# Optimization experiments

Measured on AMD Instinct MI355X. Metric: run time of the kernel, lower is better.

Reference implementation:

```python
import jax, jax.numpy as jnp
import numpy as np

T, B, D, H = 4096, 4, 1024, 16


def setup_inputs() -> dict:
    key = jax.random.key(0)
    k0, k1, k2 = jax.random.split(key, 3)
    x = jax.random.normal(k0, (T, B, D), jnp.float32)
    Wqkv = jax.random.normal(k1, (3 * D, D), jnp.float32) * 0.02
    bqkv = jnp.zeros((3 * D,), jnp.float32)
    Wout = jax.random.normal(k2, (D, D), jnp.float32) * 0.02
    bout = jnp.zeros((D,), jnp.float32)
    return {"x": x, "Wqkv": Wqkv, "bqkv": bqkv, "Wout": Wout, "bout": bout, "nhead": H}


def reference(x, Wqkv, bqkv, Wout, bout, nhead):
    # x: (T, B, D) seq-first, query is key is value
    T_, B_, D_ = x.shape
    hd = D_ // nhead
    qkv = x @ Wqkv.T + bqkv                      # (T, B, 3D)
    q, k, v = jnp.split(qkv, 3, axis=-1)         # each (T, B, D)

    def heads(t):                                 # -> (B, H, T, hd)
        return t.reshape(T_, B_, nhead, hd).transpose(1, 2, 0, 3)

    q, k, v = heads(q), heads(k), heads(v)

    # Pearson correlation over the sequence axis: X, Y are (B, H, hd, T)
    X = jnp.swapaxes(q, -2, -1)
    Y = jnp.swapaxes(k, -2, -1)
    Xc = X - X.mean(-1, keepdims=True)
    Yc = Y - Y.mean(-1, keepdims=True)
    c = jnp.einsum('bhdt,bhet->bhde', Xc, Yc)    # (B, H, hd, hd)
    sx = (Xc ** 2).sum(-1)                       # (B, H, hd)
    sy = (Yc ** 2).sum(-1)                       # (B, H, hd)
    std = jnp.sqrt(sx[..., :, None] * sy[..., None, :])
    corr = jnp.clip(c / std, -1.0, 1.0)          # (B, H, hd, hd)

    attn = jnp.einsum('bhtd,bhde->bhte', v, corr)  # v @ corr: (B, H, T, hd)
    out = attn.transpose(2, 0, 1, 3).reshape(T_, B_, D_)  # (T, B, D)
    return out @ Wout.T + bout
```

## Files before the change

### kernel.cpp

```cpp
#include <hip/hip_runtime.h>
#include <hip/hip_bf16.h>

#define TDIM 4096
#define BDIM 4
#define DDIM 1024
#define HDIM 16
#define HD   64
#define MDIM (TDIM * BDIM)

typedef __attribute__((ext_vector_type(8))) short short8v;
typedef __attribute__((ext_vector_type(4))) float f32x4;

__device__ __forceinline__ ushort f2bfu(float f) {
  union { __hip_bfloat16 h; ushort u; } c;
  c.h = __float2bfloat16(f);
  return c.u;
}
__device__ __forceinline__ float bfu2f(ushort u) {
  union { ushort u; __hip_bfloat16 h; } c;
  c.u = u;
  return __bfloat162float(c.h);
}

#define GLOAD16(gp, lp) __builtin_amdgcn_global_load_lds( \
    (const __attribute__((address_space(1))) void*)(gp),  \
    (__attribute__((address_space(3))) void*)(lp), 16, 0, 0)

#define SWZ(row) (((row) >> 1) & 3)

__global__ __launch_bounds__(256)
void split_f32(const float* __restrict__ in, ushort* __restrict__ hi,
               ushort* __restrict__ lo, int n4)
{
  int i = blockIdx.x * blockDim.x + threadIdx.x;
  const int stride = gridDim.x * blockDim.x;
  for (; i < n4; i += stride) {
    const float4 v = ((const float4*)in)[i];
    ushort4 h, l;
    h.x = f2bfu(v.x); l.x = f2bfu(v.x - bfu2f(h.x));
    h.y = f2bfu(v.y); l.y = f2bfu(v.y - bfu2f(h.y));
    h.z = f2bfu(v.z); l.z = f2bfu(v.z - bfu2f(h.z));
    h.w = f2bfu(v.w); l.w = f2bfu(v.w - bfu2f(h.w));
    ((ushort4*)hi)[i] = h;
    ((ushort4*)lo)[i] = l;
  }
}

__global__ __launch_bounds__(256, 2)
void gemm1_mfma(const float* __restrict__ X, const ushort* __restrict__ Wh,
                const ushort* __restrict__ Wl, const float* __restrict__ bias,
                float* __restrict__ Qc, float* __restrict__ Kc,
                ushort* __restrict__ Vh, ushort* __restrict__ Vl)
{
  __shared__ ushort sAh[128][32], sAl[128][32], sBh[128][32], sBl[128][32];
  const int tid = threadIdx.x;
  const int lane = tid & 63, wid = tid >> 6;
  const int m0 = blockIdx.y * 128, n0 = blockIdx.x * 128;
  const int ar = tid >> 3, aq = tid & 7;
  const int wm = wid >> 1, wn = wid & 1;
  const int fr = lane & 15, kg = lane >> 4;

  f32x4 acc[4][4];
#pragma unroll
  for (int m = 0; m < 4; ++m)
#pragma unroll
    for (int n = 0; n < 4; ++n) acc[m][n] = (f32x4){0.f, 0.f, 0.f, 0.f};

  for (int k0 = 0; k0 < DDIM; k0 += 32) {
    float4 av[4];
#pragma unroll
    for (int i = 0; i < 4; ++i)
      av[i] = *(const float4*)&X[(size_t)(m0 + ar + i * 32) * DDIM + k0 + aq * 4];
#pragma unroll
    for (int j = 0; j < 4; ++j) {
      const int c = wid * 4 + j;
      const int r0 = (c & 7) * 16;
      const int row = r0 + (lane >> 2);
      const int s = lane & 3;
      const size_t goff = (size_t)(n0 + row) * DDIM + k0 + ((s ^ SWZ(row)) << 3);
      if (c < 8) GLOAD16(Wh + goff, &sBh[r0][0]);
      else       GLOAD16(Wl + goff, &sBl[r0][0]);
    }
#pragma unroll
    for (int i = 0; i < 4; ++i) {
      const int row = ar + i * 32;
      const int sl = (((aq >> 1) ^ SWZ(row)) << 3) + ((aq & 1) << 2);
      ushort4 hv, lv;
      hv.x = f2bfu(av[i].x); lv.x = f2bfu(av[i].x - bfu2f(hv.x));
      hv.y = f2bfu(av[i].y); lv.y = f2bfu(av[i].y - bfu2f(hv.y));
      hv.z = f2bfu(av[i].z); lv.z = f2bfu(av[i].z - bfu2f(hv.z));
      hv.w = f2bfu(av[i].w); lv.w = f2bfu(av[i].w - bfu2f(hv.w));
      *(ushort4*)&sAh[row][sl] = hv;
      *(ushort4*)&sAl[row][sl] = lv;
    }
    __syncthreads();

    short8v ah[4], al[4], bh[4], bl[4];
#pragma unroll
    for (int m = 0; m < 4; ++m) {
      const int row = wm * 64 + m * 16 + fr;
      const int so = (kg ^ SWZ(row)) << 3;
      ah[m] = *(const short8v*)&sAh[row][so];
      al[m] = *(const short8v*)&sAl[row][so];
    }
#pragma unroll
    for (int n = 0; n < 4; ++n) {
      const int col = wn * 64 + n * 16 + fr;
      const int so = (kg ^ SWZ(col)) << 3;
      bh[n] = *(const short8v*)&sBh[col][so];
      bl[n] = *(const short8v*)&sBl[col][so];
    }
#pragma unroll
    for (int m = 0; m < 4; ++m)
#pragma unroll
      for (int n = 0; n < 4; ++n) {
        acc[m][n] = __builtin_amdgcn_mfma_f32_16x16x32_bf16(ah[m], bh[n], acc[m][n], 0, 0, 0);
        acc[m][n] = __builtin_amdgcn_mfma_f32_16x16x32_bf16(ah[m], bl[n], acc[m][n], 0, 0, 0);
        acc[m][n] = __builtin_amdgcn_mfma_f32_16x16x32_bf16(al[m], bh[n], acc[m][n], 0, 0, 0);
      }
    __syncthreads();
  }

  const int region = n0 >> 10;
#pragma unroll
  for (int m = 0; m < 4; ++m)
#pragma unroll
    for (int n = 0; n < 4; ++n) {
      const int col = n0 + wn * 64 + n * 16 + fr;
      const float bz = bias[col];
      const int cc = col & 1023;
      const int hh = cc >> 6, dd = cc & 63;
#pragma unroll
      for (int r = 0; r < 4; ++r) {
        const int row = m0 + wm * 64 + m * 16 + kg * 4 + r;
        const float v = acc[m][n][r] + bz;
        const int t = row >> 2, b = row & 3;
        const size_t ho = (((size_t)(b * 16 + hh)) * 4096 + t) * 64 + dd;
        if (region == 0)      Qc[ho] = v;
        else if (region == 1) Kc[ho] = v;
        else {
          const size_t o = (size_t)row * 1024 + cc;
          const ushort h2 = f2bfu(v);
          Vh[o] = h2;
          Vl[o] = f2bfu(v - bfu2f(h2));
        }
      }
    }
}

__global__ __launch_bounds__(256, 2)
void gemm2_mfma(const ushort* __restrict__ Vh, const ushort* __restrict__ Vl,
                const ushort* __restrict__ Weh, const ushort* __restrict__ Wel,
                const float* __restrict__ bias, float* __restrict__ Out)
{
  __shared__ ushort sAh[64][32], sAl[64][32], sBh[128][32], sBl[128][32];
  const int tid = threadIdx.x;
  const int lane = tid & 63, wid = tid >> 6;
  const int m0 = blockIdx.y * 64, n0 = blockIdx.x * 128, bb = blockIdx.z;
  const int wm = wid >> 1, wn = wid & 1;
  const int fr = lane & 15, kg = lane >> 4;

  f32x4 acc[2][4];
#pragma unroll
  for (int m = 0; m < 2; ++m)
#pragma unroll
    for (int n = 0; n < 4; ++n) acc[m][n] = (f32x4){0.f, 0.f, 0.f, 0.f};

  const size_t wB = (size_t)bb * DDIM * DDIM;

  for (int k0 = 0; k0 < DDIM; k0 += 32) {
#pragma unroll
    for (int j = 0; j < 6; ++j) {
      const int c = wid * 6 + j;
      const int rl = lane >> 2, s = lane & 3;
      if (c < 8) {
        const int r0 = (c & 3) * 16;
        const int row = r0 + rl;
        const size_t g = (size_t)((m0 + row) * 4 + bb) * 1024 + k0 + ((s ^ SWZ(row)) << 3);
        if (c < 4) GLOAD16(Vh + g, &sAh[r0][0]);
        else       GLOAD16(Vl + g, &sAl[r0][0]);
      } else {
        const int r0 = ((c - 8) & 7) * 16;
        const int row = r0 + rl;
        const size_t g = wB + (size_t)(n0 + row) * 1024 + k0 + ((s ^ SWZ(row)) << 3);
        if (c < 16) GLOAD16(Weh + g, &sBh[r0][0]);
        else        GLOAD16(Wel + g, &sBl[r0][0]);
      }
    }
    __syncthreads();

    short8v ah[2], al[2], bh[4], bl[4];
#pragma unroll
    for (int m = 0; m < 2; ++m) {
      const int row = wm * 32 + m * 16 + fr;
      const int so = (kg ^ SWZ(row)) << 3;
      ah[m] = *(const short8v*)&sAh[row][so];
      al[m] = *(const short8v*)&sAl[row][so];
    }
#pragma unroll
    for (int n = 0; n < 4; ++n) {
      const int col = wn * 64 + n * 16 + fr;
      const int so = (kg ^ SWZ(col)) << 3;
      bh[n] = *(const short8v*)&sBh[col][so];
      bl[n] = *(const short8v*)&sBl[col][so];
    }
#pragma unroll
    for (int m = 0; m < 2; ++m)
#pragma unroll
      for (int n = 0; n < 4; ++n) {
        acc[m][n] = __builtin_amdgcn_mfma_f32_16x16x32_bf16(ah[m], bh[n], acc[m][n], 0, 0, 0);
        acc[m][n] = __builtin_amdgcn_mfma_f32_16x16x32_bf16(ah[m], bl[n], acc[m][n], 0, 0, 0);
        acc[m][n] = __builtin_amdgcn_mfma_f32_16x16x32_bf16(al[m], bh[n], acc[m][n], 0, 0, 0);
      }
    __syncthreads();
  }

  float* Ob = Out + (size_t)bb * 1024;
#pragma unroll
  for (int m = 0; m < 2; ++m)
#pragma unroll
    for (int n = 0; n < 4; ++n) {
      const int col = n0 + wn * 64 + n * 16 + fr;
      const float bz = bias[col];
#pragma unroll
      for (int r = 0; r < 4; ++r) {
        const int row = m0 + wm * 32 + m * 16 + kg * 4 + r;
        Ob[(size_t)row * 4096 + col] = acc[m][n][r] + bz;
      }
    }
}

__global__ __launch_bounds__(256)
void corr_partial(const float* __restrict__ Qc, const float* __restrict__ Kc,
                  float* __restrict__ P)
{
  __shared__ float qs[4][16][64];
  __shared__ float ks[4][16][64];
  __shared__ float ssum[4][4][64];
  const int bh  = blockIdx.x;
  const int seg = blockIdx.y;
  const int tid = threadIdx.x;
  const int wid = tid >> 6, lane = tid & 63;
  const float* qb = Qc + (size_t)bh * 262144;
  const float* kb = Kc + (size_t)bh * 262144;
  const int ty = lane >> 3;
  const int tx = lane & 7;
  const int rr = lane >> 4;
  const int cq = lane & 15;

  float acc[8][8];
#pragma unroll
  for (int i = 0; i < 8; ++i)
#pragma unroll
    for (int j = 0; j < 8; ++j) acc[i][j] = 0.f;
  float sQ[4]  = {0,0,0,0}, sK[4]  = {0,0,0,0};
  float sQ2[4] = {0,0,0,0}, sK2[4] = {0,0,0,0};

  for (int c = 0; c < 4; ++c) {
    const int tbase = seg * 256 + wid * 64 + c * 16;
    float4 qv[4], kv[4];
#pragma unroll
    for (int i = 0; i < 4; ++i) {
      const size_t g = (size_t)(tbase + rr + i*4) * 64 + cq * 4;
      qv[i] = *(const float4*)&qb[g];
      kv[i] = *(const float4*)&kb[g];
    }
#pragma unroll
    for (int i = 0; i < 4; ++i) {
      const int row = rr + i*4;
      *(float4*)&qs[wid][row][cq*4] = qv[i];
      *(float4*)&ks[wid][row][cq*4] = kv[i];
      sQ[0] += qv[i].x; sQ[1] += qv[i].y; sQ[2] += qv[i].z; sQ[3] += qv[i].w;
      sK[0] += kv[i].x; sK[1] += kv[i].y; sK[2] += kv[i].z; sK[3] += kv[i].w;
      sQ2[0] = fmaf(qv[i].x, qv[i].x, sQ2[0]); sQ2[1] = fmaf(qv[i].y, qv[i].y, sQ2[1]);
      sQ2[2] = fmaf(qv[i].z, qv[i].z, sQ2[2]); sQ2[3] = fmaf(qv[i].w, qv[i].w, sQ2[3]);
      sK2[0] = fmaf(kv[i].x, kv[i].x, sK2[0]); sK2[1] = fmaf(kv[i].y, kv[i].y, sK2[1]);
      sK2[2] = fmaf(kv[i].z, kv[i].z, sK2[2]); sK2[3] = fmaf(kv[i].w, kv[i].w, sK2[3]);
    }
#pragma unroll 8
    for (int t = 0; t < 16; ++t) {
      const float4 qa  = *(const float4*)&qs[wid][t][ty*8];
      const float4 qb4 = *(const float4*)&qs[wid][t][ty*8+4];
      const float4 ka  = *(const float4*)&ks[wid][t][tx*8];
      const float4 kb4 = *(const float4*)&ks[wid][t][tx*8+4];
      const float av[8] = {qa.x, qa.y, qa.z, qa.w, qb4.x, qb4.y, qb4.z, qb4.w};
      const float bv[8] = {ka.x, ka.y, ka.z, ka.w, kb4.x, kb4.y, kb4.z, kb4.w};
#pragma unroll
      for (int i = 0; i < 8; ++i)
#pragma unroll
        for (int j = 0; j < 8; ++j)
          acc[i][j] = fmaf(av[i], bv[j], acc[i][j]);
    }
  }

#pragma unroll
  for (int j = 0; j < 4; ++j) {
    sQ[j]  += __shfl_xor(sQ[j], 16, 64);  sQ[j]  += __shfl_xor(sQ[j], 32, 64);
    sK[j]  += __shfl_xor(sK[j], 16, 64);  sK[j]  += __shfl_xor(sK[j], 32, 64);
    sQ2[j] += __shfl_xor(sQ2[j], 16, 64); sQ2[j] += __shfl_xor(sQ2[j], 32, 64);
    sK2[j] += __shfl_xor(sK2[j], 16, 64); sK2[j] += __shfl_xor(sK2[j], 32, 64);
  }
  if (lane < 16) {
    float4 q4; q4.x = sQ[0];  q4.y = sQ[1];  q4.z = sQ[2];  q4.w = sQ[3];
    float4 k4; k4.x = sK[0];  k4.y = sK[1];  k4.z = sK[2];  k4.w = sK[3];
    float4 q2; q2.x = sQ2[0]; q2.y = sQ2[1]; q2.z = sQ2[2]; q2.w = sQ2[3];
    float4 k2; k2.x = sK2[0]; k2.y = sK2[1]; k2.z = sK2[2]; k2.w = sK2[3];
    *(float4*)&ssum[wid][0][lane*4] = q4;
    *(float4*)&ssum[wid][1][lane*4] = k4;
    *(float4*)&ssum[wid][2][lane*4] = q2;
    *(float4*)&ssum[wid][3][lane*4] = k2;
  }

  float* cbuf = &qs[0][0][0];
  __syncthreads();
#pragma unroll
  for (int w = 0; w < 4; ++w) {
    if (wid == w) {
#pragma unroll
      for (int i = 0; i < 8; ++i) {
        float* p0 = &cbuf[(ty*8 + i) * 64 + tx*8];
        if (w == 0) {
          float4 o0, o1;
          o0.x = acc[i][0]; o0.y = acc[i][1]; o0.z = acc[i][2]; o0.w = acc[i][3];
          o1.x = acc[i][4]; o1.y = acc[i][5]; o1.z = acc[i][6]; o1.w = acc[i][7];
          *(float4*)p0 = o0; *(float4*)(p0 + 4) = o1;
        } else {
          float4 o0 = *(const float4*)p0, o1 = *(const float4*)(p0 + 4);
          o0.x += acc[i][0]; o0.y += acc[i][1]; o0.z += acc[i][2]; o0.w += acc[i][3];
          o1.x += acc[i][4]; o1.y += acc[i][5]; o1.z += acc[i][6]; o1.w += acc[i][7];
          *(float4*)p0 = o0; *(float4*)(p0 + 4) = o1;
        }
      }
    }
    __syncthreads();
  }

  float* Pb = P + (size_t)(bh * 16 + seg) * 4352;
#pragma unroll
  for (int i = 0; i < 4; ++i)
    ((float4*)Pb)[tid + 256*i] = ((const float4*)cbuf)[tid + 256*i];
  {
    const int comp = tid >> 6, d = tid & 63;
    Pb[4096 + tid] = ssum[0][comp][d] + ssum[1][comp][d] +
                     ssum[2][comp][d] + ssum[3][comp][d];
  }
}

__global__ __launch_bounds__(256)
void corr_finalize(const float* __restrict__ P, float* __restrict__ corr)
{
  __shared__ float fin[4][64];
  const int bh = blockIdx.x, qtr = blockIdx.y;
  const int tid = threadIdx.x;
  const float* Pb = P + (size_t)bh * 16 * 4352;

  float s = 0.f;
  for (int seg = 0; seg < 16; ++seg) s += Pb[(size_t)seg*4352 + 4096 + tid];
  fin[tid >> 6][tid & 63] = s;

  float cacc[4] = {0.f, 0.f, 0.f, 0.f};
  for (int seg = 0; seg < 16; ++seg) {
#pragma unroll
    for (int i = 0; i < 4; ++i)
      cacc[i] += Pb[(size_t)seg*4352 + qtr*1024 + tid + i*256];
  }
  __syncthreads();

  const float invT = 1.0f / (float)TDIM;
#pragma unroll
  for (int i = 0; i < 4; ++i) {
    const int f = qtr*1024 + tid + i*256;
    const int d = f >> 6, e = f & 63;
    const float sq = fin[0][d], sk = fin[1][e];
    const float sq2 = fin[2][d], sk2 = fin[3][e];
    const float cc = cacc[i] - sq * sk * invT;
    const float sx = sq2 - sq * sq * invT;
    const float sy = sk2 - sk * sk * invT;
    float v = cc / sqrtf(sx * sy);
    v = fminf(1.f, fmaxf(-1.f, v));
    corr[(size_t)bh * 4096 + f] = v;
  }
}

__global__ __launch_bounds__(256)
void weff_kernel(const float* __restrict__ corr, const float* __restrict__ Wout,
                 ushort* __restrict__ Weh, ushort* __restrict__ Wel)
{
  __shared__ float cs[64][64];
  __shared__ float ws[128][64];
  const int bh = blockIdx.x;
  const int b = bh >> 4, h = bh & 15;
  const int n0 = blockIdx.y * 128;
  const int tid = threadIdx.x;

  const float* cb = corr + (size_t)bh * 4096;
  float4* csv = (float4*)&cs[0][0];
#pragma unroll
  for (int i = 0; i < 4; ++i)
    csv[tid + 256*i] = ((const float4*)cb)[tid + 256*i];

  const int wr = tid >> 1, wh = (tid & 1) * 32;
  const float* wrow = Wout + (size_t)(n0 + wr) * DDIM + h * HD + wh;
#pragma unroll
  for (int i = 0; i < 8; ++i)
    *(float4*)&ws[wr][wh + i*4] = *(const float4*)&wrow[i*4];
  __syncthreads();

  const int ni = (tid >> 3) * 4;
  const int di = (tid & 7) * 8;
  float acc[4][8];
#pragma unroll
  for (int i = 0; i < 4; ++i)
#pragma unroll
    for (int j = 0; j < 8; ++j) acc[i][j] = 0.f;

  for (int e = 0; e < 64; ++e) {
    float wv[4], cv[8];
#pragma unroll
    for (int i = 0; i < 4; ++i) wv[i] = ws[ni + i][e];
#pragma unroll
    for (int j = 0; j < 8; ++j) cv[j] = cs[di + j][e];
#pragma unroll
    for (int i = 0; i < 4; ++i)
#pragma unroll
      for (int j = 0; j < 8; ++j)
        acc[i][j] = fmaf(wv[i], cv[j], acc[i][j]);
  }

  const size_t base = (size_t)b * DDIM * DDIM + h * HD;
#pragma unroll
  for (int i = 0; i < 4; ++i) {
    ushort4 h0, l0, h1, l1;
    h0.x = f2bfu(acc[i][0]); l0.x = f2bfu(acc[i][0] - bfu2f(h0.x));
    h0.y = f2bfu(acc[i][1]); l0.y = f2bfu(acc[i][1] - bfu2f(h0.y));
    h0.z = f2bfu(acc[i][2]); l0.z = f2bfu(acc[i][2] - bfu2f(h0.z));
    h0.w = f2bfu(acc[i][3]); l0.w = f2bfu(acc[i][3] - bfu2f(h0.w));
    h1.x = f2bfu(acc[i][4]); l1.x = f2bfu(acc[i][4] - bfu2f(h1.x));
    h1.y = f2bfu(acc[i][5]); l1.y = f2bfu(acc[i][5] - bfu2f(h1.y));
    h1.z = f2bfu(acc[i][6]); l1.z = f2bfu(acc[i][6] - bfu2f(h1.z));
    h1.w = f2bfu(acc[i][7]); l1.w = f2bfu(acc[i][7] - bfu2f(h1.w));
    const size_t o = base + (size_t)(n0 + ni + i) * DDIM + di;
    *(ushort4*)&Weh[o]     = h0;
    *(ushort4*)&Weh[o + 4] = h1;
    *(ushort4*)&Wel[o]     = l0;
    *(ushort4*)&Wel[o + 4] = l1;
  }
}

extern "C" void kernel_launch(void* const* d_in, const int* in_sizes, int n_in,
                              void* d_out, int out_size, void* d_ws, size_t ws_size,
                              hipStream_t stream)
{
  (void)in_sizes; (void)n_in; (void)out_size; (void)ws_size;
  const float* x    = (const float*)d_in[0];
  const float* Wqkv = (const float*)d_in[1];
  const float* bqkv = (const float*)d_in[2];
  const float* Wout = (const float*)d_in[3];
  const float* bout = (const float*)d_in[4];
  float* out = (float*)d_out;

  char* w = (char*)d_ws;
  float*  Qc    = (float*)w;   w += (size_t)67108864;
  float*  Kc    = (float*)w;   w += (size_t)67108864;
  ushort* Vh    = (ushort*)w;  w += (size_t)33554432;
  ushort* Vl    = (ushort*)w;  w += (size_t)33554432;
  float*  corrB = (float*)w;   w += (size_t)1048576;
  char* R1 = w;                w += (size_t)17825792;
  char* R2 = w;
  ushort* Wqh   = (ushort*)R1;
  ushort* Wql   = Wqh + (size_t)3145728;
  float*  P     = (float*)R1;
  ushort* Weh   = (ushort*)R2;
  ushort* Wel   = Weh + (size_t)4194304;

  split_f32<<<dim3(1024), 256, 0, stream>>>(Wqkv, Wqh, Wql, 786432);
  gemm1_mfma<<<dim3(24, 128), 256, 0, stream>>>(x, Wqh, Wql, bqkv, Qc, Kc, Vh, Vl);
  corr_partial<<<dim3(64, 16), 256, 0, stream>>>(Qc, Kc, P);
  corr_finalize<<<dim3(64, 4), 256, 0, stream>>>(P, corrB);
  weff_kernel<<<dim3(64, 8), 256, 0, stream>>>(corrB, Wout, Weh, Wel);
  gemm2_mfma<<<dim3(8, 64, 4), 256, 0, stream>>>(Vh, Vl, Weh, Wel, bout, out);
}
```

Measured before the change: 638.6 us.

## Pre-split X to bf16 hi/lo and process QKV GEMM in two halves

X is converted to bf16 hi/lo once by a separate kernel, so the first GEMM can stream A tiles straight into LDS with asynchronous global-to-LDS loads instead of loading fp32 and splitting in registers. The GEMM and correlation-partial stage now run in two halves of the sequence, reusing half-size Q/K buffers, which halves that workspace and may keep more of it cache-resident. The trailing barrier moves to the top of the k-loop. The cost is an extra pass over X in memory plus an extra kernel launch, and two serialized half-size launches.

```diff
diff --git a/kernel.cpp b/kernel.cpp
--- a/kernel.cpp
+++ b/kernel.cpp
@@ -47,16 +47,16 @@
 }
 
 __global__ __launch_bounds__(256, 2)
-void gemm1_mfma(const float* __restrict__ X, const ushort* __restrict__ Wh,
-                const ushort* __restrict__ Wl, const float* __restrict__ bias,
+void gemm1_mfma(const ushort* __restrict__ Xh, const ushort* __restrict__ Xl,
+                const ushort* __restrict__ Wh, const ushort* __restrict__ Wl,
+                const float* __restrict__ bias,
                 float* __restrict__ Qc, float* __restrict__ Kc,
-                ushort* __restrict__ Vh, ushort* __restrict__ Vl)
+                ushort* __restrict__ Vh, ushort* __restrict__ Vl, int mbase)
 {
   __shared__ ushort sAh[128][32], sAl[128][32], sBh[128][32], sBl[128][32];
   const int tid = threadIdx.x;
   const int lane = tid & 63, wid = tid >> 6;
-  const int m0 = blockIdx.y * 128, n0 = blockIdx.x * 128;
-  const int ar = tid >> 3, aq = tid & 7;
+  const int m0 = mbase + blockIdx.y * 128, n0 = blockIdx.x * 128;
   const int wm = wid >> 1, wn = wid & 1;
   const int fr = lane & 15, kg = lane >> 4;
 
@@ -67,31 +67,18 @@
     for (int n = 0; n < 4; ++n) acc[m][n] = (f32x4){0.f, 0.f, 0.f, 0.f};
 
   for (int k0 = 0; k0 < DDIM; k0 += 32) {
-    float4 av[4];
-#pragma unroll
-    for (int i = 0; i < 4; ++i)
-      av[i] = *(const float4*)&X[(size_t)(m0 + ar + i * 32) * DDIM + k0 + aq * 4];
-#pragma unroll
-    for (int j = 0; j < 4; ++j) {
-      const int c = wid * 4 + j;
+    __syncthreads();
+#pragma unroll
+    for (int j = 0; j < 8; ++j) {
+      const int c = wid * 8 + j;
       const int r0 = (c & 7) * 16;
       const int row = r0 + (lane >> 2);
       const int s = lane & 3;
-      const size_t goff = (size_t)(n0 + row) * DDIM + k0 + ((s ^ SWZ(row)) << 3);
-      if (c < 8) GLOAD16(Wh + goff, &sBh[r0][0]);
-      else       GLOAD16(Wl + goff, &sBl[r0][0]);
-    }
-#pragma unroll
-    for (int i = 0; i < 4; ++i) {
-      const int row = ar + i * 32;
-      const int sl = (((aq >> 1) ^ SWZ(row)) << 3) + ((aq & 1) << 2);
-      ushort4 hv, lv;
-      hv.x = f2bfu(av[i].x); lv.x = f2bfu(av[i].x - bfu2f(hv.x));
-      hv.y = f2bfu(av[i].y); lv.y = f2bfu(av[i].y - bfu2f(hv.y));
-      hv.z = f2bfu(av[i].z); lv.z = f2bfu(av[i].z - bfu2f(hv.z));
-      hv.w = f2bfu(av[i].w); lv.w = f2bfu(av[i].w - bfu2f(hv.w));
-      *(ushort4*)&sAh[row][sl] = hv;
-      *(ushort4*)&sAl[row][sl] = lv;
+      const int ks = k0 + ((s ^ SWZ(row)) << 3);
+      if (c < 8)       GLOAD16(Xh + (size_t)(m0 + row) * DDIM + ks, &sAh[r0][0]);
+      else if (c < 16) GLOAD16(Xl + (size_t)(m0 + row) * DDIM + ks, &sAl[r0][0]);
+      else if (c < 24) GLOAD16(Wh + (size_t)(n0 + row) * DDIM + ks, &sBh[r0][0]);
+      else             GLOAD16(Wl + (size_t)(n0 + row) * DDIM + ks, &sBl[r0][0]);
     }
     __syncthreads();
 
@@ -118,7 +105,6 @@
         acc[m][n] = __builtin_amdgcn_mfma_f32_16x16x32_bf16(ah[m], bl[n], acc[m][n], 0, 0, 0);
         acc[m][n] = __builtin_amdgcn_mfma_f32_16x16x32_bf16(al[m], bh[n], acc[m][n], 0, 0, 0);
       }
-    __syncthreads();
   }
 
   const int region = n0 >> 10;
@@ -134,8 +120,8 @@
       for (int r = 0; r < 4; ++r) {
         const int row = m0 + wm * 64 + m * 16 + kg * 4 + r;
         const float v = acc[m][n][r] + bz;
-        const int t = row >> 2, b = row & 3;
-        const size_t ho = (((size_t)(b * 16 + hh)) * 4096 + t) * 64 + dd;
+        const int tl = (row - mbase) >> 2, b = row & 3;
+        const size_t ho = (((size_t)(b * 16 + hh)) * 2048 + tl) * 64 + dd;
         if (region == 0)      Qc[ho] = v;
         else if (region == 1) Kc[ho] = v;
         else {
@@ -232,7 +218,7 @@
 
 __global__ __launch_bounds__(256)
 void corr_partial(const float* __restrict__ Qc, const float* __restrict__ Kc,
-                  float* __restrict__ P)
+                  float* __restrict__ P, int segbase)
 {
   __shared__ float qs[4][16][64];
   __shared__ float ks[4][16][64];
@@ -241,8 +227,8 @@
   const int seg = blockIdx.y;
   const int tid = threadIdx.x;
   const int wid = tid >> 6, lane = tid & 63;
-  const float* qb = Qc + (size_t)bh * 262144;
-  const float* kb = Kc + (size_t)bh * 262144;
+  const float* qb = Qc + (size_t)bh * 131072;
+  const float* kb = Kc + (size_t)bh * 131072;
   const int ty = lane >> 3;
   const int tx = lane & 7;
   const int rr = lane >> 4;
@@ -335,7 +321,7 @@
     __syncthreads();
   }
 
-  float* Pb = P + (size_t)(bh * 16 + seg) * 4352;
+  float* Pb = P + (size_t)(bh * 16 + segbase + seg) * 4352;
 #pragma unroll
   for (int i = 0; i < 4; ++i)
     ((float4*)Pb)[tid + 256*i] = ((const float4*)cbuf)[tid + 256*i];
@@ -460,22 +446,28 @@
   float* out = (float*)d_out;
 
   char* w = (char*)d_ws;
-  float*  Qc    = (float*)w;   w += (size_t)67108864;
-  float*  Kc    = (float*)w;   w += (size_t)67108864;
+  ushort* Xh    = (ushort*)w;  w += (size_t)33554432;
+  ushort* Xl    = (ushort*)w;  w += (size_t)33554432;
+  float*  Qch   = (float*)w;   w += (size_t)33554432;
+  float*  Kch   = (float*)w;   w += (size_t)33554432;
   ushort* Vh    = (ushort*)w;  w += (size_t)33554432;
   ushort* Vl    = (ushort*)w;  w += (size_t)33554432;
   float*  corrB = (float*)w;   w += (size_t)1048576;
-  char* R1 = w;                w += (size_t)17825792;
+  float*  P     = (float*)w;   w += (size_t)17825792;
   char* R2 = w;
-  ushort* Wqh   = (ushort*)R1;
+  ushort* Wqh   = (ushort*)R2;
   ushort* Wql   = Wqh + (size_t)3145728;
-  float*  P     = (float*)R1;
   ushort* Weh   = (ushort*)R2;
   ushort* Wel   = Weh + (size_t)4194304;
 
+  split_f32<<<dim3(2048), 256, 0, stream>>>(x, Xh, Xl, 4194304);
   split_f32<<<dim3(1024), 256, 0, stream>>>(Wqkv, Wqh, Wql, 786432);
-  gemm1_mfma<<<dim3(24, 128), 256, 0, stream>>>(x, Wqh, Wql, bqkv, Qc, Kc, Vh, Vl);
-  corr_partial<<<dim3(64, 16), 256, 0, stream>>>(Qc, Kc, P);
+  gemm1_mfma<<<dim3(24, 64), 256, 0, stream>>>(Xh, Xl, Wqh, Wql, bqkv,
+                                               Qch, Kch, Vh, Vl, 0);
+  corr_partial<<<dim3(64, 8), 256, 0, stream>>>(Qch, Kch, P, 0);
+  gemm1_mfma<<<dim3(24, 64), 256, 0, stream>>>(Xh, Xl, Wqh, Wql, bqkv,
+                                               Qch, Kch, Vh, Vl, 8192);
+  corr_partial<<<dim3(64, 8), 256, 0, stream>>>(Qch, Kch, P, 8);
   corr_finalize<<<dim3(64, 4), 256, 0, stream>>>(P, corrB);
   weff_kernel<<<dim3(64, 8), 256, 0, stream>>>(corrB, Wout, Weh, Wel);
   gemm2_mfma<<<dim3(8, 64, 4), 256, 0, stream>>>(Vh, Vl, Weh, Wel, bout, out);
```

Result: slower. 705.1 us (+10.4%).

## Double-buffer LDS tiles in QKV projection GEMM to overlap loads with MFMA

Applied to the files above, without the earlier changes.

The QKV projection GEMM now keeps two LDS buffers for the A (split bf16 hi/lo) and B tiles. It issues the global-to-LDS loads and X register loads for the next k-step before running the MFMAs on the current buffer, then converts and stores the next A tile afterwards. This drops one barrier per iteration and hides global memory latency behind compute. In exchange it doubles LDS use to 64KB per block, which may limit the two blocks per CU requested by launch bounds, and raises register pressure from the prefetched float4 values.

```diff
diff --git a/kernel.cpp b/kernel.cpp
--- a/kernel.cpp
+++ b/kernel.cpp
@@ -52,7 +52,8 @@
                 float* __restrict__ Qc, float* __restrict__ Kc,
                 ushort* __restrict__ Vh, ushort* __restrict__ Vl)
 {
-  __shared__ ushort sAh[128][32], sAl[128][32], sBh[128][32], sBl[128][32];
+  __shared__ ushort sAh[2][128][32], sAl[2][128][32];
+  __shared__ ushort sBh[2][128][32], sBl[2][128][32];
   const int tid = threadIdx.x;
   const int lane = tid & 63, wid = tid >> 6;
   const int m0 = blockIdx.y * 128, n0 = blockIdx.x * 128;
@@ -66,20 +67,20 @@
 #pragma unroll
     for (int n = 0; n < 4; ++n) acc[m][n] = (f32x4){0.f, 0.f, 0.f, 0.f};
 
-  for (int k0 = 0; k0 < DDIM; k0 += 32) {
+  {
     float4 av[4];
 #pragma unroll
     for (int i = 0; i < 4; ++i)
-      av[i] = *(const float4*)&X[(size_t)(m0 + ar + i * 32) * DDIM + k0 + aq * 4];
+      av[i] = *(const float4*)&X[(size_t)(m0 + ar + i * 32) * DDIM + aq * 4];
 #pragma unroll
     for (int j = 0; j < 4; ++j) {
       const int c = wid * 4 + j;
       const int r0 = (c & 7) * 16;
       const int row = r0 + (lane >> 2);
       const int s = lane & 3;
-      const size_t goff = (size_t)(n0 + row) * DDIM + k0 + ((s ^ SWZ(row)) << 3);
-      if (c < 8) GLOAD16(Wh + goff, &sBh[r0][0]);
-      else       GLOAD16(Wl + goff, &sBl[r0][0]);
+      const size_t goff = (size_t)(n0 + row) * DDIM + ((s ^ SWZ(row)) << 3);
+      if (c < 8) GLOAD16(Wh + goff, &sBh[0][r0][0]);
+      else       GLOAD16(Wl + goff, &sBl[0][r0][0]);
     }
 #pragma unroll
     for (int i = 0; i < 4; ++i) {
@@ -90,25 +91,47 @@
       hv.y = f2bfu(av[i].y); lv.y = f2bfu(av[i].y - bfu2f(hv.y));
       hv.z = f2bfu(av[i].z); lv.z = f2bfu(av[i].z - bfu2f(hv.z));
       hv.w = f2bfu(av[i].w); lv.w = f2bfu(av[i].w - bfu2f(hv.w));
-      *(ushort4*)&sAh[row][sl] = hv;
-      *(ushort4*)&sAl[row][sl] = lv;
+      *(ushort4*)&sAh[0][row][sl] = hv;
+      *(ushort4*)&sAl[0][row][sl] = lv;
     }
     __syncthreads();
+  }
+
+  int cur = 0;
+  for (int k0 = 0; k0 < DDIM; k0 += 32) {
+    const int nxt = cur ^ 1;
+    const bool has_next = (k0 + 32 < DDIM);
+    float4 av[4];
+    if (has_next) {
+#pragma unroll
+      for (int j = 0; j < 4; ++j) {
+        const int c = wid * 4 + j;
+        const int r0 = (c & 7) * 16;
+        const int row = r0 + (lane >> 2);
+        const int s = lane & 3;
+        const size_t goff = (size_t)(n0 + row) * DDIM + k0 + 32 + ((s ^ SWZ(row)) << 3);
+        if (c < 8) GLOAD16(Wh + goff, &sBh[nxt][r0][0]);
+        else       GLOAD16(Wl + goff, &sBl[nxt][r0][0]);
+      }
+#pragma unroll
+      for (int i = 0; i < 4; ++i)
+        av[i] = *(const float4*)&X[(size_t)(m0 + ar + i * 32) * DDIM + k0 + 32 + aq * 4];
+    }
 
     short8v ah[4], al[4], bh[4], bl[4];
 #pragma unroll
     for (int m = 0; m < 4; ++m) {
       const int row = wm * 64 + m * 16 + fr;
       const int so = (kg ^ SWZ(row)) << 3;
-      ah[m] = *(const short8v*)&sAh[row][so];
-      al[m] = *(const short8v*)&sAl[row][so];
+      ah[m] = *(const short8v*)&sAh[cur][row][so];
+      al[m] = *(const short8v*)&sAl[cur][row][so];
     }
 #pragma unroll
     for (int n = 0; n < 4; ++n) {
       const int col = wn * 64 + n * 16 + fr;
       const int so = (kg ^ SWZ(col)) << 3;
-      bh[n] = *(const short8v*)&sBh[col][so];
-      bl[n] = *(const short8v*)&sBl[col][so];
+      bh[n] = *(const short8v*)&sBh[cur][col][so];
+      bl[n] = *(const short8v*)&sBl[cur][col][so];
     }
 #pragma unroll
     for (int m = 0; m < 4; ++m)
@@ -118,7 +141,23 @@
         acc[m][n] = __builtin_amdgcn_mfma_f32_16x16x32_bf16(ah[m], bl[n], acc[m][n], 0, 0, 0);
         acc[m][n] = __builtin_amdgcn_mfma_f32_16x16x32_bf16(al[m], bh[n], acc[m][n], 0, 0, 0);
       }
+
+    if (has_next) {
+#pragma unroll
+      for (int i = 0; i < 4; ++i) {
+        const int row = ar + i * 32;
+        const int sl = (((aq >> 1) ^ SWZ(row)) << 3) + ((aq & 1) << 2);
+        ushort4 hv, lv;
+        hv.x = f2bfu(av[i].x); lv.x = f2bfu(av[i].x - bfu2f(hv.x));
+        hv.y = f2bfu(av[i].y); lv.y = f2bfu(av[i].y - bfu2f(hv.y));
+        hv.z = f2bfu(av[i].z); lv.z = f2bfu(av[i].z - bfu2f(hv.z));
+        hv.w = f2bfu(av[i].w); lv.w = f2bfu(av[i].w - bfu2f(hv.w));
+        *(ushort4*)&sAh[nxt][row][sl] = hv;
+        *(ushort4*)&sAl[nxt][row][sl] = lv;
+      }
+    }
     __syncthreads();
+    cur = nxt;
   }
 
   const int region = n0 >> 10;
```

After: 665.8 us. 4.3% more time.

## Fold V projection into per-batch output weight to skip V materialization

Applied to the files above, without the earlier changes.

Stops computing and storing V in the first GEMM. Instead the value projection weight is composed with the per-batch effective output weight (Wout·corr), giving a fused per-batch weight Wfull and bias. The final GEMM then reads x directly, with a 128-row tile and on-the-fly bf16 hi/lo splitting. This removes a third of GEMM1's work and the V write/read round trip, at the cost of an extra 4×1024³ weight-composition GEMM, a small serial bias kernel, and an extra rounding step in the fused weights.

```diff
diff --git a/kernel.cpp b/kernel.cpp
--- a/kernel.cpp
+++ b/kernel.cpp
@@ -46,11 +46,42 @@
   }
 }
 
+__global__ __launch_bounds__(256)
+void wvt_split(const float* __restrict__ Wqkv, ushort* __restrict__ WvTh,
+               ushort* __restrict__ WvTl)
+{
+  __shared__ float ld[64][68];
+  const int d0 = blockIdx.x * 64, e0 = blockIdx.y * 64;
+  const int tid = threadIdx.x;
+  const int rr = tid >> 4, cc = tid & 15;
+#pragma unroll
+  for (int i = 0; i < 4; ++i) {
+    const int el = rr + i * 16;
+    const float4 v = *(const float4*)&Wqkv[(size_t)(2048 + e0 + el) * 1024 + d0 + cc * 4];
+    ld[el][cc*4+0] = v.x; ld[el][cc*4+1] = v.y;
+    ld[el][cc*4+2] = v.z; ld[el][cc*4+3] = v.w;
+  }
+  __syncthreads();
+#pragma unroll
+  for (int i = 0; i < 4; ++i) {
+    const int dl = rr + i * 16;
+    const float v0 = ld[cc*4+0][dl], v1 = ld[cc*4+1][dl];
+    const float v2 = ld[cc*4+2][dl], v3 = ld[cc*4+3][dl];
+    ushort4 h4, l4;
+    h4.x = f2bfu(v0); l4.x = f2bfu(v0 - bfu2f(h4.x));
+    h4.y = f2bfu(v1); l4.y = f2bfu(v1 - bfu2f(h4.y));
+    h4.z = f2bfu(v2); l4.z = f2bfu(v2 - bfu2f(h4.z));
+    h4.w = f2bfu(v3); l4.w = f2bfu(v3 - bfu2f(h4.w));
+    const size_t o = (size_t)(d0 + dl) * 1024 + e0 + cc * 4;
+    *(ushort4*)&WvTh[o] = h4;
+    *(ushort4*)&WvTl[o] = l4;
+  }
+}
+
 __global__ __launch_bounds__(256, 2)
-void gemm1_mfma(const float* __restrict__ X, const ushort* __restrict__ Wh,
-                const ushort* __restrict__ Wl, const float* __restrict__ bias,
-                float* __restrict__ Qc, float* __restrict__ Kc,
-                ushort* __restrict__ Vh, ushort* __restrict__ Vl)
+void gemm1_qk(const float* __restrict__ X, const ushort* __restrict__ Wh,
+              const ushort* __restrict__ Wl, const float* __restrict__ bias,
+              float* __restrict__ Qc, float* __restrict__ Kc)
 {
   __shared__ ushort sAh[128][32], sAl[128][32], sBh[128][32], sBl[128][32];
   const int tid = threadIdx.x;
@@ -136,22 +167,16 @@
         const float v = acc[m][n][r] + bz;
         const int t = row >> 2, b = row & 3;
         const size_t ho = (((size_t)(b * 16 + hh)) * 4096 + t) * 64 + dd;
-        if (region == 0)      Qc[ho] = v;
-        else if (region == 1) Kc[ho] = v;
-        else {
-          const size_t o = (size_t)row * 1024 + cc;
-          const ushort h2 = f2bfu(v);
-          Vh[o] = h2;
-          Vl[o] = f2bfu(v - bfu2f(h2));
-        }
+        if (region == 0) Qc[ho] = v;
+        else             Kc[ho] = v;
       }
     }
 }
 
 __global__ __launch_bounds__(256, 2)
-void gemm2_mfma(const ushort* __restrict__ Vh, const ushort* __restrict__ Vl,
-                const ushort* __restrict__ Weh, const ushort* __restrict__ Wel,
-                const float* __restrict__ bias, float* __restrict__ Out)
+void wfull_mfma(const ushort* __restrict__ Aeh, const ushort* __restrict__ Ael,
+                const ushort* __restrict__ Bth, const ushort* __restrict__ Btl,
+                ushort* __restrict__ Wfh, ushort* __restrict__ Wfl)
 {
   __shared__ ushort sAh[64][32], sAl[64][32], sBh[128][32], sBl[128][32];
   const int tid = threadIdx.x;
@@ -166,7 +191,7 @@
 #pragma unroll
     for (int n = 0; n < 4; ++n) acc[m][n] = (f32x4){0.f, 0.f, 0.f, 0.f};
 
-  const size_t wB = (size_t)bb * DDIM * DDIM;
+  const size_t aB = (size_t)bb * 1048576;
 
   for (int k0 = 0; k0 < DDIM; k0 += 32) {
 #pragma unroll
@@ -176,15 +201,15 @@
       if (c < 8) {
         const int r0 = (c & 3) * 16;
         const int row = r0 + rl;
-        const size_t g = (size_t)((m0 + row) * 4 + bb) * 1024 + k0 + ((s ^ SWZ(row)) << 3);
-        if (c < 4) GLOAD16(Vh + g, &sAh[r0][0]);
-        else       GLOAD16(Vl + g, &sAl[r0][0]);
+        const size_t g = aB + (size_t)(m0 + row) * 1024 + k0 + ((s ^ SWZ(row)) << 3);
+        if (c < 4) GLOAD16(Aeh + g, &sAh[r0][0]);
+        else       GLOAD16(Ael + g, &sAl[r0][0]);
       } else {
         const int r0 = ((c - 8) & 7) * 16;
         const int row = r0 + rl;
-        const size_t g = wB + (size_t)(n0 + row) * 1024 + k0 + ((s ^ SWZ(row)) << 3);
-        if (c < 16) GLOAD16(Weh + g, &sBh[r0][0]);
-        else        GLOAD16(Wel + g, &sBl[r0][0]);
+        const size_t g = (size_t)(n0 + row) * 1024 + k0 + ((s ^ SWZ(row)) << 3);
+        if (c < 16) GLOAD16(Bth + g, &sBh[r0][0]);
+        else        GLOAD16(Btl + g, &sBl[r0][0]);
       }
     }
     __syncthreads();
@@ -215,16 +240,137 @@
     __syncthreads();
   }
 
-  float* Ob = Out + (size_t)bb * 1024;
 #pragma unroll
   for (int m = 0; m < 2; ++m)
 #pragma unroll
     for (int n = 0; n < 4; ++n) {
       const int col = n0 + wn * 64 + n * 16 + fr;
-      const float bz = bias[col];
 #pragma unroll
       for (int r = 0; r < 4; ++r) {
         const int row = m0 + wm * 32 + m * 16 + kg * 4 + r;
+        const float v = acc[m][n][r];
+        const size_t o = aB + (size_t)row * 1024 + col;
+        const ushort h2 = f2bfu(v);
+        Wfh[o] = h2;
+        Wfl[o] = f2bfu(v - bfu2f(h2));
+      }
+    }
+}
+
+__global__ __launch_bounds__(256)
+void bias2_kernel(const ushort* __restrict__ Weh, const ushort* __restrict__ Wel,
+                  const float* __restrict__ bqkv, const float* __restrict__ bout,
+                  float* __restrict__ bias2)
+{
+  __shared__ float bvs[1024];
+  const int b = blockIdx.x, tid = threadIdx.x;
+  *(float4*)&bvs[tid * 4] = *(const float4*)&bqkv[2048 + tid * 4];
+  __syncthreads();
+  const size_t base = (size_t)b * 1048576;
+#pragma unroll
+  for (int j = 0; j < 4; ++j) {
+    const int n = tid + j * 256;
+    const ushort* hr = Weh + base + (size_t)n * 1024;
+    const ushort* lr = Wel + base + (size_t)n * 1024;
+    float s = 0.f;
+    for (int e = 0; e < 1024; e += 4) {
+      const ushort4 h4 = *(const ushort4*)&hr[e];
+      const ushort4 l4 = *(const ushort4*)&lr[e];
+      s += (bfu2f(h4.x) + bfu2f(l4.x)) * bvs[e]
+         + (bfu2f(h4.y) + bfu2f(l4.y)) * bvs[e + 1]
+         + (bfu2f(h4.z) + bfu2f(l4.z)) * bvs[e + 2]
+         + (bfu2f(h4.w) + bfu2f(l4.w)) * bvs[e + 3];
+    }
+    bias2[b * 1024 + n] = s + bout[n];
+  }
+}
+
+__global__ __launch_bounds__(256, 2)
+void gemm2x(const float* __restrict__ X, const ushort* __restrict__ Bh_,
+            const ushort* __restrict__ Bl_, const float* __restrict__ bias2,
+            float* __restrict__ Out)
+{
+  __shared__ ushort sAh[128][32], sAl[128][32], sBh[128][32], sBl[128][32];
+  const int tid = threadIdx.x;
+  const int lane = tid & 63, wid = tid >> 6;
+  const int m0 = blockIdx.y * 128, n0 = blockIdx.x * 128, bb = blockIdx.z;
+  const int ar = tid >> 3, aq = tid & 7;
+  const int wm = wid >> 1, wn = wid & 1;
+  const int fr = lane & 15, kg = lane >> 4;
+
+  f32x4 acc[4][4];
+#pragma unroll
+  for (int m = 0; m < 4; ++m)
+#pragma unroll
+    for (int n = 0; n < 4; ++n) acc[m][n] = (f32x4){0.f, 0.f, 0.f, 0.f};
+
+  const size_t wB = (size_t)bb * 1048576;
+
+  for (int k0 = 0; k0 < DDIM; k0 += 32) {
+    float4 av[4];
+#pragma unroll
+    for (int i = 0; i < 4; ++i)
+      av[i] = *(const float4*)&X[((size_t)((m0 + ar + i * 32) * 4 + bb)) * 1024 + k0 + aq * 4];
+#pragma unroll
+    for (int j = 0; j < 4; ++j) {
+      const int c = wid * 4 + j;
+      const int r0 = (c & 7) * 16;
+      const int row = r0 + (lane >> 2);
+      const int s = lane & 3;
+      const size_t goff = wB + (size_t)(n0 + row) * 1024 + k0 + ((s ^ SWZ(row)) << 3);
+      if (c < 8) GLOAD16(Bh_ + goff, &sBh[r0][0]);
+      else       GLOAD16(Bl_ + goff, &sBl[r0][0]);
+    }
+#pragma unroll
+    for (int i = 0; i < 4; ++i) {
+      const int row = ar + i * 32;
+      const int sl = (((aq >> 1) ^ SWZ(row)) << 3) + ((aq & 1) << 2);
+      ushort4 hv, lv;
+      hv.x = f2bfu(av[i].x); lv.x = f2bfu(av[i].x - bfu2f(hv.x));
+      hv.y = f2bfu(av[i].y); lv.y = f2bfu(av[i].y - bfu2f(hv.y));
+      hv.z = f2bfu(av[i].z); lv.z = f2bfu(av[i].z - bfu2f(hv.z));
+      hv.w = f2bfu(av[i].w); lv.w = f2bfu(av[i].w - bfu2f(hv.w));
+      *(ushort4*)&sAh[row][sl] = hv;
+      *(ushort4*)&sAl[row][sl] = lv;
+    }
+    __syncthreads();
+
+    short8v ah[4], al[4], bh[4], bl[4];
+#pragma unroll
+    for (int m = 0; m < 4; ++m) {
+      const int row = wm * 64 + m * 16 + fr;
+      const int so = (kg ^ SWZ(row)) << 3;
+      ah[m] = *(const short8v*)&sAh[row][so];
+      al[m] = *(const short8v*)&sAl[row][so];
+    }
+#pragma unroll
+    for (int n = 0; n < 4; ++n) {
+      const int col = wn * 64 + n * 16 + fr;
+      const int so = (kg ^ SWZ(col)) << 3;
+      bh[n] = *(const short8v*)&sBh[col][so];
+      bl[n] = *(const short8v*)&sBl[col][so];
+    }
+#pragma unroll
+    for (int m = 0; m < 4; ++m)
+#pragma unroll
+      for (int n = 0; n < 4; ++n) {
+        acc[m][n] = __builtin_amdgcn_mfma_f32_16x16x32_bf16(ah[m], bh[n], acc[m][n], 0, 0, 0);
+        acc[m][n] = __builtin_amdgcn_mfma_f32_16x16x32_bf16(ah[m], bl[n], acc[m][n], 0, 0, 0);
+        acc[m][n] = __builtin_amdgcn_mfma_f32_16x16x32_bf16(al[m], bh[n], acc[m][n], 0, 0, 0);
+      }
+    __syncthreads();
+  }
+
+  float* Ob = Out + (size_t)bb * 1024;
+#pragma unroll
+  for (int m = 0; m < 4; ++m)
+#pragma unroll
+    for (int n = 0; n < 4; ++n) {
+      const int col = n0 + wn * 64 + n * 16 + fr;
+      const float bz = bias2[bb * 1024 + col];
+#pragma unroll
+      for (int r = 0; r < 4; ++r) {
+        const int row = m0 + wm * 64 + m * 16 + kg * 4 + r;
         Ob[(size_t)row * 4096 + col] = acc[m][n][r] + bz;
       }
     }
@@ -462,21 +608,26 @@
   char* w = (char*)d_ws;
   float*  Qc    = (float*)w;   w += (size_t)67108864;
   float*  Kc    = (float*)w;   w += (size_t)67108864;
-  ushort* Vh    = (ushort*)w;  w += (size_t)33554432;
-  ushort* Vl    = (ushort*)w;  w += (size_t)33554432;
   float*  corrB = (float*)w;   w += (size_t)1048576;
   char* R1 = w;                w += (size_t)17825792;
-  char* R2 = w;
+  ushort* Weh   = (ushort*)w;  w += (size_t)8388608;
+  ushort* Wel   = (ushort*)w;  w += (size_t)8388608;
+  ushort* WvTh  = (ushort*)w;  w += (size_t)2097152;
+  ushort* WvTl  = (ushort*)w;  w += (size_t)2097152;
+  ushort* Wfh   = (ushort*)w;  w += (size_t)8388608;
+  ushort* Wfl   = (ushort*)w;  w += (size_t)8388608;
+  float*  bias2 = (float*)w;   w += (size_t)16384;
   ushort* Wqh   = (ushort*)R1;
-  ushort* Wql   = Wqh + (size_t)3145728;
+  ushort* Wql   = Wqh + (size_t)2097152;
   float*  P     = (float*)R1;
-  ushort* Weh   = (ushort*)R2;
-  ushort* Wel   = Weh + (size_t)4194304;
-
-  split_f32<<<dim3(1024), 256, 0, stream>>>(Wqkv, Wqh, Wql, 786432);
-  gemm1_mfma<<<dim3(24, 128), 256, 0, stream>>>(x, Wqh, Wql, bqkv, Qc, Kc, Vh, Vl);
+
+  split_f32<<<dim3(1024), 256, 0, stream>>>(Wqkv, Wqh, Wql, 524288);
+  wvt_split<<<dim3(16, 16), 256, 0, stream>>>(Wqkv, WvTh, WvTl);
+  gemm1_qk<<<dim3(16, 128), 256, 0, stream>>>(x, Wqh, Wql, bqkv, Qc, Kc);
   corr_partial<<<dim3(64, 16), 256, 0, stream>>>(Qc, Kc, P);
   corr_finalize<<<dim3(64, 4), 256, 0, stream>>>(P, corrB);
   weff_kernel<<<dim3(64, 8), 256, 0, stream>>>(corrB, Wout, Weh, Wel);
-  gemm2_mfma<<<dim3(8, 64, 4), 256, 0, stream>>>(Vh, Vl, Weh, Wel, bout, out);
-}
+  wfull_mfma<<<dim3(8, 16, 4), 256, 0, stream>>>(Weh, Wel, WvTh, WvTl, Wfh, Wfl);
+  bias2_kernel<<<dim3(4), 256, 0, stream>>>(Weh, Wel, bqkv, bout, bias2);
+  gemm2x<<<dim3(8, 32, 4), 256, 0, stream>>>(x, Wfh, Wfl, bias2, out);
+}
```

Result: slower. 682.1 us (+6.8%).
